# Optimization experiments

Measured on AMD Instinct MI355X. Metric: run time of the kernel, lower is better.

The kernel has to match this reference:

```python
import jax, jax.numpy as jnp
import numpy as np
import math

D_MODEL = 768
H = 12
D_FF = 3072
HEAD_DIM = D_MODEL // H
EPS = 1e-5


def setup_inputs() -> dict:
    key = jax.random.key(0)
    ks = jax.random.split(key, 12)
    s = 1.0 / math.sqrt(D_MODEL)
    inp = {
        "x": jax.random.normal(ks[0], (8, 1024, D_MODEL), dtype=jnp.float32),
        # attention projections (stored as [d_in, d_out])
        "wq": jax.random.normal(ks[1], (D_MODEL, D_MODEL), jnp.float32) * s,
        "bq": jnp.zeros((D_MODEL,), jnp.float32),
        "wk": jax.random.normal(ks[2], (D_MODEL, D_MODEL), jnp.float32) * s,
        "bk": jnp.zeros((D_MODEL,), jnp.float32),
        "wv": jax.random.normal(ks[3], (D_MODEL, D_MODEL), jnp.float32) * s,
        "bv": jnp.zeros((D_MODEL,), jnp.float32),
        "wo": jax.random.normal(ks[4], (D_MODEL, D_MODEL), jnp.float32) * s,
        "bo": jnp.zeros((D_MODEL,), jnp.float32),
        # FFN
        "w1": jax.random.normal(ks[5], (D_MODEL, D_FF), jnp.float32) * s,
        "b1": jnp.zeros((D_FF,), jnp.float32),
        "w2": jax.random.normal(ks[6], (D_FF, D_MODEL), jnp.float32) * (1.0 / math.sqrt(D_FF)),
        "b2": jnp.zeros((D_MODEL,), jnp.float32),
        # LayerNormalization scalar params (gemma/beta) for the two residual norms
        "g1": jnp.ones((1,), jnp.float32),
        "be1": jnp.zeros((1,), jnp.float32),
        "g2": jnp.ones((1,), jnp.float32),
        "be2": jnp.zeros((1,), jnp.float32),
    }
    return inp


def _layernorm(x, g, b):
    # torch: mean and UNBIASED std over last dim; divide by (std + eps)
    mean = jnp.mean(x, axis=-1, keepdims=True)
    std = jnp.std(x, axis=-1, keepdims=True, ddof=1)
    return g * (x - mean) / (std + EPS) + b


def _attention(x, wq, bq, wk, bk, wv, bv, wo, bo):
    B, N, _ = x.shape
    q = (x @ wq + bq).reshape(B, N, H, HEAD_DIM)
    k = (x @ wk + bk).reshape(B, N, H, HEAD_DIM)
    v = (x @ wv + bv).reshape(B, N, H, HEAD_DIM)
    scores = jnp.einsum("bqhd,bkhd->bhqk", q, k) / math.sqrt(HEAD_DIM)
    w = jax.nn.softmax(scores, axis=-1)
    out = jnp.einsum("bhqk,bkhd->bqhd", w, v).reshape(B, N, D_MODEL)
    return out @ wo + bo


def _ffn(x, w1, b1, w2, b2):
    return (jax.nn.gelu(x @ w1 + b1, approximate=False)) @ w2 + b2


def reference(x, wq, bq, wk, bk, wv, bv, wo, bo, w1, b1, w2, b2, g1, be1, g2, be2):
    # pre-LN residual block 1: attention
    x = x + _attention(_layernorm(x, g1, be1), wq, bq, wk, bk, wv, bv, wo, bo)
    # pre-LN residual block 2: FFN
    x = x + _ffn(_layernorm(x, g2, be2), w1, b1, w2, b2)
    return x
```

## Files before the change

kernel.cpp:

```cpp
#include <hip/hip_runtime.h>
#include <hip/hip_bf16.h>
#include <math.h>

typedef unsigned short u16;
typedef unsigned int u32;
typedef u16 u16x8 __attribute__((ext_vector_type(8)));
typedef __bf16 bf16x8 __attribute__((ext_vector_type(8)));
typedef float f32x4 __attribute__((ext_vector_type(4)));

#define MODE_GELU 1
#define MODE_RESF32 2
#define MODE_QKV 3

template <typename T, typename F>
__device__ __forceinline__ T bitcast(F f) { return __builtin_bit_cast(T, f); }

__device__ __forceinline__ u16 f2bf(float f) {
    unsigned int u = __float_as_uint(f);
    u = (u + 0x7fffu + ((u >> 16) & 1u)) >> 16;
    return (u16)u;
}

__device__ __forceinline__ u32 packbf(float lo, float hi) {
    return (u32)f2bf(lo) | ((u32)f2bf(hi) << 16);
}

__device__ __forceinline__ float fast_gelu(float x) {
    const float arg = x * (2.30220775f + 0.10294329f * x * x);
    const float e = exp2f(arg);
    return x * (1.0f - __builtin_amdgcn_rcpf(e + 1.0f));
}

__device__ __forceinline__ void gl_lds16(const u16* g, u16* l) {
    __builtin_amdgcn_global_load_lds(
        (const __attribute__((address_space(1))) unsigned int*)(const void*)g,
        (__attribute__((address_space(3))) unsigned int*)(void*)l,
        16, 0, 0);
}

__device__ __forceinline__ void stage64(const u16* __restrict__ src, int stride,
                                        u16* __restrict__ lds, int t)
{
    const int wave = t >> 6, lane = t & 63;
#pragma unroll
    for (int i = 0; i < 2; i++) {
        const int row = i * 32 + wave * 8 + (lane >> 3);
        const int s = lane & 7;
        const int f = (((row >> 3) & 1) << 2) | (row & 3);
        gl_lds16(src + (size_t)row * stride + (size_t)((s ^ f) << 3),
                 lds + i * 2048 + wave * 512);
    }
}

__device__ __forceinline__ void stage64w8(const u16* __restrict__ src, int stride,
                                          u16* __restrict__ lds, int t)
{
    const int wave = t >> 6, lane = t & 63;
    const int row = wave * 8 + (lane >> 3);
    const int s = lane & 7;
    const int f = (((row >> 3) & 1) << 2) | (row & 3);
    gl_lds16(src + (size_t)row * stride + (size_t)((s ^ f) << 3),
             lds + wave * 512);
}

__global__ __launch_bounds__(256) void prep_kernel(
    const float* __restrict__ wq, const float* __restrict__ wk,
    const float* __restrict__ wv, const float* __restrict__ wo,
    const float* __restrict__ w1, const float* __restrict__ w2,
    const float* __restrict__ bq, const float* __restrict__ bk,
    const float* __restrict__ bv,
    u16* __restrict__ wqkvT, u16* __restrict__ woT,
    u16* __restrict__ w1T, u16* __restrict__ w2T, float* __restrict__ bqkv,
    const float* __restrict__ X, u16* __restrict__ Y,
    const float* __restrict__ gp, const float* __restrict__ bp)
{
    const int blk = blockIdx.x;
    if (blk >= 6921) {
        __shared__ float sbuf[8];
        const int row = blk - 6921, t = threadIdx.x;
        const float* xr = X + (size_t)row * 768;
        float v0 = xr[t], v1 = xr[t + 256], v2 = xr[t + 512];
        float s = v0 + v1 + v2;
        float q = v0 * v0 + v1 * v1 + v2 * v2;
#pragma unroll
        for (int m = 1; m < 64; m <<= 1) {
            s += __shfl_xor(s, m, 64);
            q += __shfl_xor(q, m, 64);
        }
        const int wave = t >> 6, lane = t & 63;
        if (lane == 0) { sbuf[wave] = s; sbuf[4 + wave] = q; }
        __syncthreads();
        s = sbuf[0] + sbuf[1] + sbuf[2] + sbuf[3];
        q = sbuf[4] + sbuf[5] + sbuf[6] + sbuf[7];
        const float mean = s * (1.0f / 768.0f);
        float ssd = fmaxf(q - 768.0f * mean * mean, 0.0f);
        const float stdv = sqrtf(ssd * (1.0f / 767.0f));
        const float scale = gp[0] / (stdv + 1e-5f);
        const float beta = bp[0];
        u16* yr = Y + (size_t)row * 768;
        yr[t]       = f2bf((v0 - mean) * scale + beta);
        yr[t + 256] = f2bf((v1 - mean) * scale + beta);
        yr[t + 512] = f2bf((v2 - mean) * scale + beta);
        return;
    }
    if (blk >= 6912) {
        const int t = (blk - 6912) * 256 + threadIdx.x;
        if (t < 2304)
            bqkv[t] = t < 768 ? bq[t] : (t < 1536 ? bk[t - 768] : bv[t - 1536]);
        return;
    }
    const float* W; u16* WT; int Krows, Ncols, lt;
    if (blk < 576)       { W = wq; WT = wqkvT;                       Krows = 768;  Ncols = 768;  lt = blk; }
    else if (blk < 1152) { W = wk; WT = wqkvT + (size_t)768 * 768;   Krows = 768;  Ncols = 768;  lt = blk - 576; }
    else if (blk < 1728) { W = wv; WT = wqkvT + (size_t)1536 * 768;  Krows = 768;  Ncols = 768;  lt = blk - 1152; }
    else if (blk < 2304) { W = wo; WT = woT;                         Krows = 768;  Ncols = 768;  lt = blk - 1728; }
    else if (blk < 4608) { W = w1; WT = w1T;                         Krows = 768;  Ncols = 3072; lt = blk - 2304; }
    else                 { W = w2; WT = w2T;                         Krows = 3072; Ncols = 768;  lt = blk - 4608; }
    const int ktiles = Krows >> 5;
    const int k0 = (lt % ktiles) * 32, n0 = (lt / ktiles) * 32;

    __shared__ float tile[32][33];
    const int tx = threadIdx.x & 31, ty = threadIdx.x >> 5;
#pragma unroll
    for (int j = 0; j < 32; j += 8)
        tile[ty + j][tx] = W[(size_t)(k0 + ty + j) * Ncols + n0 + tx];
    __syncthreads();
#pragma unroll
    for (int j = 0; j < 32; j += 8)
        WT[(size_t)(n0 + ty + j) * Krows + k0 + tx] = f2bf(tile[tx][ty + j]);
}

__global__ __launch_bounds__(256) void ln_kernel(
    const float* __restrict__ X, u16* __restrict__ Y,
    const float* __restrict__ gp, const float* __restrict__ bp)
{
    __shared__ float sbuf[8];
    const int row = blockIdx.x, t = threadIdx.x;
    const float* xr = X + (size_t)row * 768;
    float v0 = xr[t], v1 = xr[t + 256], v2 = xr[t + 512];
    float s = v0 + v1 + v2;
    float q = v0 * v0 + v1 * v1 + v2 * v2;
#pragma unroll
    for (int m = 1; m < 64; m <<= 1) {
        s += __shfl_xor(s, m, 64);
        q += __shfl_xor(q, m, 64);
    }
    const int wave = t >> 6, lane = t & 63;
    if (lane == 0) { sbuf[wave] = s; sbuf[4 + wave] = q; }
    __syncthreads();
    s = sbuf[0] + sbuf[1] + sbuf[2] + sbuf[3];
    q = sbuf[4] + sbuf[5] + sbuf[6] + sbuf[7];
    const float mean = s * (1.0f / 768.0f);
    float ssd = fmaxf(q - 768.0f * mean * mean, 0.0f);
    const float stdv = sqrtf(ssd * (1.0f / 767.0f));
    const float scale = gp[0] / (stdv + 1e-5f);
    const float beta = bp[0];
    u16* yr = Y + (size_t)row * 768;
    yr[t]       = f2bf((v0 - mean) * scale + beta);
    yr[t + 256] = f2bf((v1 - mean) * scale + beta);
    yr[t + 512] = f2bf((v2 - mean) * scale + beta);
}

template <int MODE>
__global__ __launch_bounds__(256) void gemm_kernel(
    const u16* __restrict__ A, const u16* __restrict__ BT,
    const float* __restrict__ bias, const float* __restrict__ res,
    void* __restrict__ out0, void* __restrict__ out1, void* __restrict__ out2,
    int M, int N, int K)
{
    __shared__ u16 sh[2][2][128 * 64];
    u16* shp = &sh[0][0][0];
    const int t = threadIdx.x;
    const int lane = t & 63, wave = t >> 6;
    const int wr = wave >> 1, wc = wave & 1;
    const int g = lane >> 4, c = lane & 15;

    const int lin = blockIdx.x + blockIdx.y * gridDim.x;
    const int xcd = lin & 7, idx = lin >> 3;
    const int bm = xcd * 8 + (idx & 7);
    const int bn = idx >> 3;

    const int srow = wave * 32 + (lane >> 3);
    const u16* Ag = A + (size_t)(bm * 128 + srow) * K;
    const u16* Bg = BT + (size_t)(bn * 128 + srow) * K;

    const int fc = (((c >> 3) & 1) << 2) | (c & 3);
    const int xs0 = (g ^ fc) << 3;
    const int xs1 = ((4 + g) ^ fc) << 3;

    f32x4 acc[4][4] = {};
    const int nk = K >> 6;

    const int sl = lane & 7;
    int sco[4];
#pragma unroll
    for (int it = 0; it < 4; it++)
        sco[it] = ((sl ^ (((it & 1) << 2) | ((lane >> 3) & 3))) << 3);

#define STAGE_AB(buf, k0)                                                     \
    {                                                                         \
        _Pragma("unroll")                                                     \
        for (int it = 0; it < 4; it++) {                                      \
            gl_lds16(Ag + (size_t)(it * 8) * K + (k0) + sco[it], &sh[buf][0][wave * 2048 + it * 512]); \
            gl_lds16(Bg + (size_t)(it * 8) * K + (k0) + sco[it], &sh[buf][1][wave * 2048 + it * 512]); \
        }                                                                     \
    }

    STAGE_AB(0, 0);
    __syncthreads();

    for (int ks = 0; ks < nk; ks++) {
        const int cur = ks & 1;
        if (ks + 1 < nk) STAGE_AB(cur ^ 1, (ks + 1) << 6);
        const u16* Asb = sh[cur][0];
        const u16* Bsb = sh[cur][1];
        __builtin_amdgcn_s_setprio(1);
#pragma unroll
        for (int kk = 0; kk < 2; kk++) {
            const int xo = kk ? xs1 : xs0;
            bf16x8 af[4], bfr[4];
#pragma unroll
            for (int m = 0; m < 4; m++)
                af[m] = *(const bf16x8*)&Asb[(wr * 64 + m * 16 + c) * 64 + xo];
#pragma unroll
            for (int n = 0; n < 4; n++)
                bfr[n] = *(const bf16x8*)&Bsb[(wc * 64 + n * 16 + c) * 64 + xo];
#pragma unroll
            for (int m = 0; m < 4; m++)
#pragma unroll
                for (int n = 0; n < 4; n++)
                    acc[m][n] = __builtin_amdgcn_mfma_f32_16x16x32_bf16(
                        af[m], bfr[n], acc[m][n], 0, 0, 0);
        }
        __builtin_amdgcn_s_setprio(0);
        __syncthreads();
    }
#undef STAGE_AB

    if constexpr (MODE == MODE_QKV) {
        if (bn >= 12) {
#pragma unroll
            for (int m = 0; m < 4; m++) {
#pragma unroll
                for (int n = 0; n < 4; n++) {
                    const int colL = wc * 64 + n * 16 + c;
                    const int rowLb = wr * 64 + m * 16 + 4 * g;
                    const float bv = bias[bn * 128 + colL];
                    const u32 x0 = packbf(acc[m][n][0] + bv, acc[m][n][1] + bv);
                    const u32 x1 = packbf(acc[m][n][2] + bv, acc[m][n][3] + bv);
                    const int elem = colL * 128 + (rowLb ^ ((colL & 15) << 3));
                    ((u32*)shp)[elem >> 1] = x0;
                    ((u32*)shp)[(elem >> 1) + 1] = x1;
                }
            }
            __syncthreads();
            const int bn_off = bn - 12;
            const int bb = bm >> 3, kvb = (bm & 7) * 128;
            const int j8 = (t & 7) * 8;
#pragma unroll
            for (int it = 0; it < 4; it++) {
                const int colL2 = it * 32 + (t >> 3);
                const int gcol = bn_off * 128 + colL2;
                const int hh = gcol >> 6, d = gcol & 63;
                const size_t obase = ((size_t)(bb * 12 + hh) << 16) + ((size_t)d << 10) + kvb;
                const int X = (colL2 & 15) << 3;
#pragma unroll
                for (int half = 0; half < 2; half++) {
                    const int rowL2 = half * 64 + j8;
                    const int elem = colL2 * 128 + (rowL2 ^ X);
                    *(u16x8*)((u16*)out2 + obase + rowL2) = *(const u16x8*)&shp[elem];
                }
            }
            return;
        }
    }

#pragma unroll
    for (int m = 0; m < 4; m++) {
        const int row = bm * 128 + wr * 64 + m * 16 + 4 * g;
#pragma unroll
        for (int n = 0; n < 4; n++) {
            const int col = bn * 128 + wc * 64 + n * 16 + c;
            const float bv = bias[col];
#pragma unroll
            for (int i = 0; i < 4; i++) {
                float v = acc[m][n][i] + bv;
                if constexpr (MODE == MODE_GELU) {
                    ((u16*)out0)[(size_t)(row + i) * N + col] = f2bf(fast_gelu(v));
                } else if constexpr (MODE == MODE_RESF32) {
                    const size_t idx = (size_t)(row + i) * N + col;
                    ((float*)out0)[idx] = v + res[idx];
                } else {
                    const int sect = (col >= 768) ? 1 : 0;
                    const int colm = col - sect * 768;
                    u16* dst = sect ? (u16*)out1 : (u16*)out0;
                    dst[(size_t)(row + i) * 768 + colm] = f2bf(v);
                }
            }
        }
    }
}

__global__ __launch_bounds__(256) void gemm64_kernel(
    const u16* __restrict__ A, const u16* __restrict__ BT,
    const float* __restrict__ bias, const float* __restrict__ res,
    float* __restrict__ out0, int M, int N, int K)
{
    __shared__ u16 sh[2][3][64 * 64];
    const int t = threadIdx.x;
    const int lane = t & 63, wave = t >> 6;
    const int g = lane >> 4, c = lane & 15;

    const int lin = blockIdx.x + blockIdx.y * gridDim.x;
    const int xcd = lin & 7, idx = lin >> 3;
    const int bm = xcd * 16 + (idx & 15);
    const int bn = idx >> 4;

    const u16* Ag = A + (size_t)(bm * 64) * K;
    const u16* Bg = BT + (size_t)(bn * 128) * K;

    const int fc = (((c >> 3) & 1) << 2) | (c & 3);
    const int xs0 = (g ^ fc) << 3;
    const int xs1 = ((4 + g) ^ fc) << 3;

    f32x4 acc[4][2] = {};
    const int nk = K >> 6;

#define STAGE64_AB(buf, k0)                                                   \
    {                                                                         \
        stage64(Ag + (k0), K, &sh[buf][0][0], t);                             \
        stage64(Bg + (k0), K, &sh[buf][1][0], t);                             \
        stage64(Bg + (size_t)64 * K + (k0), K, &sh[buf][2][0], t);            \
    }

    STAGE64_AB(0, 0);
    __syncthreads();

    for (int ks = 0; ks < nk; ks++) {
        const int cur = ks & 1;
        if (ks + 1 < nk) STAGE64_AB(cur ^ 1, (ks + 1) << 6);
        const u16* Asb = sh[cur][0];
        const u16* Bb = sh[cur][1 + (wave >> 1)];
        const int brow = (wave & 1) * 32;
        __builtin_amdgcn_s_setprio(1);
#pragma unroll
        for (int kk = 0; kk < 2; kk++) {
            const int xo = kk ? xs1 : xs0;
            bf16x8 af[4], bfr[2];
#pragma unroll
            for (int m = 0; m < 4; m++)
                af[m] = *(const bf16x8*)&Asb[(m * 16 + c) * 64 + xo];
#pragma unroll
            for (int n = 0; n < 2; n++)
                bfr[n] = *(const bf16x8*)&Bb[(brow + n * 16 + c) * 64 + xo];
#pragma unroll
            for (int m = 0; m < 4; m++)
#pragma unroll
                for (int n = 0; n < 2; n++)
                    acc[m][n] = __builtin_amdgcn_mfma_f32_16x16x32_bf16(
                        af[m], bfr[n], acc[m][n], 0, 0, 0);
        }
        __builtin_amdgcn_s_setprio(0);
        __syncthreads();
    }
#undef STAGE64_AB

#pragma unroll
    for (int m = 0; m < 4; m++) {
        const int row = bm * 64 + m * 16 + 4 * g;
#pragma unroll
        for (int n = 0; n < 2; n++) {
            const int col = bn * 128 + wave * 32 + n * 16 + c;
            const float bv = bias[col];
#pragma unroll
            for (int i = 0; i < 4; i++) {
                const size_t idxo = (size_t)(row + i) * N + col;
                out0[idxo] = acc[m][n][i] + bv + res[idxo];
            }
        }
    }
}

__global__ __launch_bounds__(512) void attn_kernel(
    const u16* __restrict__ Qg, const u16* __restrict__ Kg,
    const u16* __restrict__ Vt_g, u16* __restrict__ O)
{
    __shared__ u16 Kl[2][4096];
    __shared__ u16 Vl[2][4096];
    const int t = threadIdx.x, lane = t & 63, wave = t >> 6;
    const int g = lane >> 4, c = lane & 15;
    const int l = blockIdx.x;
    const int pos = l >> 3;
    const int b = l & 7, h = pos >> 3;
    const int qt = pos & 7;
    const int bh = b * 12 + h;
    const size_t rowb = (size_t)b * 1024;
    const int q0 = qt * 128 + wave * 16;

    bf16x8 qa[2];
    {
        const u16* qp = Qg + (rowb + q0 + c) * 768 + h * 64 + g * 8;
        u16x8 a0 = *(const u16x8*)qp;
        u16x8 a1 = *(const u16x8*)(qp + 32);
        bf16x8 va0, va1;
#pragma unroll
        for (int j = 0; j < 8; j++) {
            const float SC = 0.18033688011112042f;
            va0[j] = (__bf16)(__uint_as_float(((u32)a0[j]) << 16) * SC);
            va1[j] = (__bf16)(__uint_as_float(((u32)a1[j]) << 16) * SC);
        }
        qa[0] = va0; qa[1] = va1;
    }

    bf16x8 vone;
#pragma unroll
    for (int j = 0; j < 8; j++) vone[j] = (__bf16)1.0f;

    int kro[4], kxo[4], vro[4];
#pragma unroll
    for (int n = 0; n < 4; n++) {
        const int pr = ((n >> 1) << 5) + ((c >> 2) << 3) + ((n & 1) << 2) + (c & 3);
        kro[n] = pr << 6;
        kxo[n] = (((pr >> 3) & 1) << 2) | (pr & 3);
        vro[n] = (n * 16 + c) << 6;
    }
    const int vxo = (((c >> 3) & 1) << 2) | (c & 3);

    const u16* ksrc = Kg + rowb * 768 + h * 64;
    const u16* vsrc = Vt_g + (size_t)bh * 65536;

    f32x4 oa[4] = {};
    f32x4 lsum = {};

    stage64w8(ksrc, 768, Kl[0], t);
    stage64w8(vsrc, 1024, Vl[0], t);
    __syncthreads();

    for (int kvt = 0; kvt < 16; ++kvt) {
        const u16* Kc = Kl[kvt & 1];
        const u16* Vc = Vl[kvt & 1];
        if (kvt < 15) {
            stage64w8(ksrc + (size_t)(kvt + 1) * 64 * 768, 768, Kl[(kvt + 1) & 1], t);
            stage64w8(vsrc + (kvt + 1) * 64, 1024, Vl[(kvt + 1) & 1], t);
        }

        f32x4 s0[4] = {};
        __builtin_amdgcn_s_setprio(1);
#pragma unroll
        for (int n = 0; n < 4; n++) {
#pragma unroll
            for (int kk = 0; kk < 2; kk++) {
                const bf16x8 kf = *(const bf16x8*)&Kc[kro[n] + ((((kk << 2) + g) ^ kxo[n]) << 3)];
                s0[n] = __builtin_amdgcn_mfma_f32_16x16x32_bf16(kf, qa[kk], s0[n], 0, 0, 0);
            }
        }
        __builtin_amdgcn_s_setprio(0);

        bf16x8 pa00, pa01;
#pragma unroll
        for (int n = 0; n < 4; n++)
#pragma unroll
            for (int i = 0; i < 4; i++)
                s0[n][i] = exp2f(fminf(s0[n][i], 60.0f));
#pragma unroll
        for (int i = 0; i < 4; i++) {
            pa00[i] = (__bf16)s0[0][i]; pa00[4 + i] = (__bf16)s0[1][i];
            pa01[i] = (__bf16)s0[2][i]; pa01[4 + i] = (__bf16)s0[3][i];
        }

        __builtin_amdgcn_s_setprio(1);
        lsum = __builtin_amdgcn_mfma_f32_16x16x32_bf16(pa00, vone, lsum, 0, 0, 0);
        lsum = __builtin_amdgcn_mfma_f32_16x16x32_bf16(pa01, vone, lsum, 0, 0, 0);
#pragma unroll
        for (int n = 0; n < 4; n++) {
#pragma unroll
            for (int kk = 0; kk < 2; kk++) {
                const bf16x8 vf = *(const bf16x8*)&Vc[vro[n] + ((((kk << 2) + g) ^ vxo) << 3)];
                oa[n] = __builtin_amdgcn_mfma_f32_16x16x32_bf16(kk ? pa01 : pa00, vf, oa[n], 0, 0, 0);
            }
        }
        __builtin_amdgcn_s_setprio(0);
        __syncthreads();
    }

#pragma unroll
    for (int i = 0; i < 4; i++) {
        const float ia_ = 1.0f / fmaxf(lsum[i], 1e-30f);
        const size_t ra_ = rowb + q0 + 4 * g + i;
#pragma unroll
        for (int n = 0; n < 4; n++)
            O[ra_ * 768 + h * 64 + n * 16 + c] = f2bf(oa[n][i] * ia_);
    }
}

extern "C" void kernel_launch(void* const* d_in, const int* in_sizes, int n_in,
                              void* d_out, int out_size, void* d_ws, size_t ws_size,
                              hipStream_t stream)
{
    const float* x   = (const float*)d_in[0];
    const float* wq  = (const float*)d_in[1];
    const float* bq  = (const float*)d_in[2];
    const float* wk  = (const float*)d_in[3];
    const float* bk  = (const float*)d_in[4];
    const float* wv  = (const float*)d_in[5];
    const float* bv  = (const float*)d_in[6];
    const float* wo  = (const float*)d_in[7];
    const float* bo  = (const float*)d_in[8];
    const float* w1  = (const float*)d_in[9];
    const float* b1  = (const float*)d_in[10];
    const float* w2  = (const float*)d_in[11];
    const float* b2  = (const float*)d_in[12];
    const float* g1  = (const float*)d_in[13];
    const float* be1 = (const float*)d_in[14];
    const float* g2  = (const float*)d_in[15];
    const float* be2 = (const float*)d_in[16];

    char* ws = (char*)d_ws;
    constexpr size_t O_WQKV = 0;
    constexpr size_t O_WO   = 3538944;
    constexpr size_t O_W1   = 4718592;
    constexpr size_t O_W2   = 9437184;
    constexpr size_t O_BQKV = 14155776;
    constexpr size_t O_XLN  = 14168064;
    constexpr size_t O_Q    = O_XLN + 12582912;
    constexpr size_t O_K    = O_Q + 12582912;
    constexpr size_t O_VT   = O_K + 12582912;
    constexpr size_t O_ATTN = O_VT + 12582912;
    constexpr size_t O_H    = O_ATTN + 12582912;
    constexpr size_t O_F    = O_XLN;
    constexpr size_t O_HLN  = O_ATTN;

    u16* wqkvT = (u16*)(ws + O_WQKV);
    u16* woT   = (u16*)(ws + O_WO);
    u16* w1T   = (u16*)(ws + O_W1);
    u16* w2T   = (u16*)(ws + O_W2);
    float* bqkv = (float*)(ws + O_BQKV);
    u16* xln   = (u16*)(ws + O_XLN);
    u16* Qb    = (u16*)(ws + O_Q);
    u16* Kb    = (u16*)(ws + O_K);
    u16* VTg   = (u16*)(ws + O_VT);
    u16* attnb = (u16*)(ws + O_ATTN);
    float* h   = (float*)(ws + O_H);
    u16* fb    = (u16*)(ws + O_F);
    u16* hln   = (u16*)(ws + O_HLN);

    dim3 blk(256);
    prep_kernel<<<6921 + 8192, blk, 0, stream>>>(wq, wk, wv, wo, w1, w2, bq, bk, bv,
                                                 wqkvT, woT, w1T, w2T, bqkv,
                                                 x, xln, g1, be1);
    gemm_kernel<MODE_QKV><<<dim3(64, 18), blk, 0, stream>>>(
        xln, wqkvT, bqkv, nullptr, Qb, Kb, VTg, 8192, 2304, 768);
    attn_kernel<<<768, dim3(512), 0, stream>>>(Qb, Kb, VTg, attnb);
    gemm64_kernel<<<dim3(128, 6), blk, 0, stream>>>(
        attnb, woT, bo, x, h, 8192, 768, 768);
    ln_kernel<<<8192, blk, 0, stream>>>(h, hln, g2, be2);
    gemm_kernel<MODE_GELU><<<dim3(64, 24), blk, 0, stream>>>(
        hln, w1T, b1, nullptr, fb, nullptr, nullptr, 8192, 3072, 768);
    gemm64_kernel<<<dim3(128, 6), blk, 0, stream>>>(
        fb, w2T, b2, h, (float*)d_out, 8192, 768, 3072);
}
```

Measured before the change: 227.4 us.

## Use 8-wave 128x128 GEMM tiles and store residual intermediate in bf16

The 128x128 GEMM for QKV and FFN1 now runs with 512 threads (8 waves in a 2x4 layout), each wave owning a 64x32 sub-tile instead of 64x64. This halves accumulator registers per wave and doubles the waves available to hide latency, and the global-to-LDS staging loop is reorganised to match. Separately, the post-attention residual h is stored as bf16 instead of fp32, so LayerNorm 2 and the final residual add read half the bytes. This adds rounding error to the residual path.

```diff
diff --git a/kernel.cpp b/kernel.cpp
--- a/kernel.cpp
+++ b/kernel.cpp
@@ -9,7 +9,6 @@
 typedef float f32x4 __attribute__((ext_vector_type(4)));
 
 #define MODE_GELU 1
-#define MODE_RESF32 2
 #define MODE_QKV 3
 
 template <typename T, typename F>
@@ -19,6 +18,10 @@
     unsigned int u = __float_as_uint(f);
     u = (u + 0x7fffu + ((u >> 16) & 1u)) >> 16;
     return (u16)u;
+}
+
+__device__ __forceinline__ float bf2f(u16 u) {
+    return __uint_as_float(((u32)u) << 16);
 }
 
 __device__ __forceinline__ u32 packbf(float lo, float hi) {
@@ -130,14 +133,14 @@
         WT[(size_t)(n0 + ty + j) * Krows + k0 + tx] = f2bf(tile[tx][ty + j]);
 }
 
-__global__ __launch_bounds__(256) void ln_kernel(
-    const float* __restrict__ X, u16* __restrict__ Y,
+__global__ __launch_bounds__(256) void ln_bf16_kernel(
+    const u16* __restrict__ X, u16* __restrict__ Y,
     const float* __restrict__ gp, const float* __restrict__ bp)
 {
     __shared__ float sbuf[8];
     const int row = blockIdx.x, t = threadIdx.x;
-    const float* xr = X + (size_t)row * 768;
-    float v0 = xr[t], v1 = xr[t + 256], v2 = xr[t + 512];
+    const u16* xr = X + (size_t)row * 768;
+    float v0 = bf2f(xr[t]), v1 = bf2f(xr[t + 256]), v2 = bf2f(xr[t + 512]);
     float s = v0 + v1 + v2;
     float q = v0 * v0 + v1 * v1 + v2 * v2;
 #pragma unroll
@@ -162,9 +165,9 @@
 }
 
 template <int MODE>
-__global__ __launch_bounds__(256) void gemm_kernel(
+__global__ __launch_bounds__(512) void gemm8w_kernel(
     const u16* __restrict__ A, const u16* __restrict__ BT,
-    const float* __restrict__ bias, const float* __restrict__ res,
+    const float* __restrict__ bias,
     void* __restrict__ out0, void* __restrict__ out1, void* __restrict__ out2,
     int M, int N, int K)
 {
@@ -172,7 +175,7 @@
     u16* shp = &sh[0][0][0];
     const int t = threadIdx.x;
     const int lane = t & 63, wave = t >> 6;
-    const int wr = wave >> 1, wc = wave & 1;
+    const int wr = wave >> 2, wc = wave & 3;
     const int g = lane >> 4, c = lane & 15;
 
     const int lin = blockIdx.x + blockIdx.y * gridDim.x;
@@ -180,70 +183,66 @@
     const int bm = xcd * 8 + (idx & 7);
     const int bn = idx >> 3;
 
-    const int srow = wave * 32 + (lane >> 3);
-    const u16* Ag = A + (size_t)(bm * 128 + srow) * K;
-    const u16* Bg = BT + (size_t)(bn * 128 + srow) * K;
+    const int srow = t >> 3;
+    const int sf = (((t >> 6) & 1) << 2) | ((t >> 3) & 3);
+    const int sxor = ((t & 7) ^ sf) << 3;
+    const u16* Ag = A + (size_t)(bm * 128 + srow) * K + sxor;
+    const u16* Bg = BT + (size_t)(bn * 128 + srow) * K + sxor;
 
     const int fc = (((c >> 3) & 1) << 2) | (c & 3);
     const int xs0 = (g ^ fc) << 3;
     const int xs1 = ((4 + g) ^ fc) << 3;
 
-    f32x4 acc[4][4] = {};
+    f32x4 acc[4][2] = {};
     const int nk = K >> 6;
 
-    const int sl = lane & 7;
-    int sco[4];
-#pragma unroll
-    for (int it = 0; it < 4; it++)
-        sco[it] = ((sl ^ (((it & 1) << 2) | ((lane >> 3) & 3))) << 3);
-
-#define STAGE_AB(buf, k0)                                                     \
+#define STAGE8(buf, k0)                                                       \
     {                                                                         \
         _Pragma("unroll")                                                     \
-        for (int it = 0; it < 4; it++) {                                      \
-            gl_lds16(Ag + (size_t)(it * 8) * K + (k0) + sco[it], &sh[buf][0][wave * 2048 + it * 512]); \
-            gl_lds16(Bg + (size_t)(it * 8) * K + (k0) + sco[it], &sh[buf][1][wave * 2048 + it * 512]); \
+        for (int i = 0; i < 2; i++) {                                         \
+            gl_lds16(Ag + (size_t)(i * 64) * K + (k0), &sh[buf][0][i * 4096 + wave * 512]); \
+            gl_lds16(Bg + (size_t)(i * 64) * K + (k0), &sh[buf][1][i * 4096 + wave * 512]); \
         }                                                                     \
     }
 
-    STAGE_AB(0, 0);
+    STAGE8(0, 0);
     __syncthreads();
 
     for (int ks = 0; ks < nk; ks++) {
         const int cur = ks & 1;
-        if (ks + 1 < nk) STAGE_AB(cur ^ 1, (ks + 1) << 6);
+        if (ks + 1 < nk) STAGE8(cur ^ 1, (ks + 1) << 6);
         const u16* Asb = sh[cur][0];
         const u16* Bsb = sh[cur][1];
         __builtin_amdgcn_s_setprio(1);
 #pragma unroll
         for (int kk = 0; kk < 2; kk++) {
             const int xo = kk ? xs1 : xs0;
-            bf16x8 af[4], bfr[4];
+            bf16x8 af[4], bfr[2];
 #pragma unroll
             for (int m = 0; m < 4; m++)
                 af[m] = *(const bf16x8*)&Asb[(wr * 64 + m * 16 + c) * 64 + xo];
 #pragma unroll
-            for (int n = 0; n < 4; n++)
-                bfr[n] = *(const bf16x8*)&Bsb[(wc * 64 + n * 16 + c) * 64 + xo];
+            for (int n = 0; n < 2; n++)
+                bfr[n] = *(const bf16x8*)&Bsb[(wc * 32 + n * 16 + c) * 64 + xo];
 #pragma unroll
             for (int m = 0; m < 4; m++)
 #pragma unroll
-                for (int n = 0; n < 4; n++)
+                for (int n = 0; n < 2; n++)
                     acc[m][n] = __builtin_amdgcn_mfma_f32_16x16x32_bf16(
                         af[m], bfr[n], acc[m][n], 0, 0, 0);
         }
         __builtin_amdgcn_s_setprio(0);
         __syncthreads();
     }
-#undef STAGE_AB
+#undef STAGE8
 
     if constexpr (MODE == MODE_QKV) {
         if (bn >= 12) {
 #pragma unroll
             for (int m = 0; m < 4; m++) {
 #pragma unroll
-                for (int n = 0; n < 4; n++) {
-                    const int colL = wc * 64 + n * 16 + c;
+                for (int n = 0; n < 2; n++) {
+                    const int colL = wc * 32 + n * 16 + c;
                     const int rowLb = wr * 64 + m * 16 + 4 * g;
                     const float bv = bias[bn * 128 + colL];
                     const u32 x0 = packbf(acc[m][n][0] + bv, acc[m][n][1] + bv);
@@ -258,8 +257,8 @@
             const int bb = bm >> 3, kvb = (bm & 7) * 128;
             const int j8 = (t & 7) * 8;
 #pragma unroll
-            for (int it = 0; it < 4; it++) {
-                const int colL2 = it * 32 + (t >> 3);
+            for (int it = 0; it < 2; it++) {
+                const int colL2 = it * 64 + (t >> 3);
                 const int gcol = bn_off * 128 + colL2;
                 const int hh = gcol >> 6, d = gcol & 63;
                 const size_t obase = ((size_t)(bb * 12 + hh) << 16) + ((size_t)d << 10) + kvb;
@@ -279,17 +278,14 @@
     for (int m = 0; m < 4; m++) {
         const int row = bm * 128 + wr * 64 + m * 16 + 4 * g;
 #pragma unroll
-        for (int n = 0; n < 4; n++) {
-            const int col = bn * 128 + wc * 64 + n * 16 + c;
+        for (int n = 0; n < 2; n++) {
+            const int col = bn * 128 + wc * 32 + n * 16 + c;
             const float bv = bias[col];
 #pragma unroll
             for (int i = 0; i < 4; i++) {
                 float v = acc[m][n][i] + bv;
                 if constexpr (MODE == MODE_GELU) {
                     ((u16*)out0)[(size_t)(row + i) * N + col] = f2bf(fast_gelu(v));
-                } else if constexpr (MODE == MODE_RESF32) {
-                    const size_t idx = (size_t)(row + i) * N + col;
-                    ((float*)out0)[idx] = v + res[idx];
                 } else {
                     const int sect = (col >= 768) ? 1 : 0;
                     const int colm = col - sect * 768;
@@ -301,10 +297,11 @@
     }
 }
 
+template <int RES_BF16>
 __global__ __launch_bounds__(256) void gemm64_kernel(
     const u16* __restrict__ A, const u16* __restrict__ BT,
-    const float* __restrict__ bias, const float* __restrict__ res,
-    float* __restrict__ out0, int M, int N, int K)
+    const float* __restrict__ bias, const void* __restrict__ res,
+    void* __restrict__ out0, int M, int N, int K)
 {
     __shared__ u16 sh[2][3][64 * 64];
     const int t = threadIdx.x;
@@ -375,7 +372,13 @@
 #pragma unroll
             for (int i = 0; i < 4; i++) {
                 const size_t idxo = (size_t)(row + i) * N + col;
-                out0[idxo] = acc[m][n][i] + bv + res[idxo];
+                if constexpr (RES_BF16 == 0) {
+                    const float r = ((const float*)res)[idxo];
+                    ((u16*)out0)[idxo] = f2bf(acc[m][n][i] + bv + r);
+                } else {
+                    const float r = bf2f(((const u16*)res)[idxo]);
+                    ((float*)out0)[idxo] = acc[m][n][i] + bv + r;
+                }
             }
         }
     }
@@ -406,8 +409,8 @@
 #pragma unroll
         for (int j = 0; j < 8; j++) {
             const float SC = 0.18033688011112042f;
-            va0[j] = (__bf16)(__uint_as_float(((u32)a0[j]) << 16) * SC);
-            va1[j] = (__bf16)(__uint_as_float(((u32)a1[j]) << 16) * SC);
+            va0[j] = (__bf16)(bf2f(a0[j]) * SC);
+            va1[j] = (__bf16)(bf2f(a1[j]) * SC);
         }
         qa[0] = va0; qa[1] = va1;
     }
@@ -540,7 +543,7 @@
     u16* Kb    = (u16*)(ws + O_K);
     u16* VTg   = (u16*)(ws + O_VT);
     u16* attnb = (u16*)(ws + O_ATTN);
-    float* h   = (float*)(ws + O_H);
+    u16* hB    = (u16*)(ws + O_H);
     u16* fb    = (u16*)(ws + O_F);
     u16* hln   = (u16*)(ws + O_HLN);
 
@@ -548,14 +551,14 @@
     prep_kernel<<<6921 + 8192, blk, 0, stream>>>(wq, wk, wv, wo, w1, w2, bq, bk, bv,
                                                  wqkvT, woT, w1T, w2T, bqkv,
                                                  x, xln, g1, be1);
-    gemm_kernel<MODE_QKV><<<dim3(64, 18), blk, 0, stream>>>(
-        xln, wqkvT, bqkv, nullptr, Qb, Kb, VTg, 8192, 2304, 768);
+    gemm8w_kernel<MODE_QKV><<<dim3(64, 18), dim3(512), 0, stream>>>(
+        xln, wqkvT, bqkv, Qb, Kb, VTg, 8192, 2304, 768);
     attn_kernel<<<768, dim3(512), 0, stream>>>(Qb, Kb, VTg, attnb);
-    gemm64_kernel<<<dim3(128, 6), blk, 0, stream>>>(
-        attnb, woT, bo, x, h, 8192, 768, 768);
-    ln_kernel<<<8192, blk, 0, stream>>>(h, hln, g2, be2);
-    gemm_kernel<MODE_GELU><<<dim3(64, 24), blk, 0, stream>>>(
-        hln, w1T, b1, nullptr, fb, nullptr, nullptr, 8192, 3072, 768);
-    gemm64_kernel<<<dim3(128, 6), blk, 0, stream>>>(
-        fb, w2T, b2, h, (float*)d_out, 8192, 768, 3072);
-}
+    gemm64_kernel<0><<<dim3(128, 6), blk, 0, stream>>>(
+        attnb, woT, bo, x, hB, 8192, 768, 768);
+    ln_bf16_kernel<<<8192, blk, 0, stream>>>(hB, hln, g2, be2);
+    gemm8w_kernel<MODE_GELU><<<dim3(64, 24), dim3(512), 0, stream>>>(
+        hln, w1T, b1, fb, nullptr, nullptr, 8192, 3072, 768);
+    gemm64_kernel<1><<<dim3(128, 6), blk, 0, stream>>>(
+        fb, w2T, b2, hB, (float*)d_out, 8192, 768, 3072);
+}
```

Result: no change. 228.5 us (median of 3 runs) (+0.4%).
